# Optimization experiments

Measured on AMD Instinct MI355X. Metric: run time of the kernel, lower is better.

The kernel has to match this reference:

```python
import jax, jax.numpy as jnp
import numpy as np

IN_F, OUT_F, EDGE_D = 128, 128, 16
B, S, E = 16, 1024, 8192
T = 1.0
NEG_SLOPE = 0.2


def setup_inputs() -> dict:
    key = jax.random.key(0)
    k1, k2, k3, k4, k5 = jax.random.split(key, 5)
    x = jax.random.normal(k1, (B, S, IN_F), dtype=jnp.float32)
    edge_index = jax.random.randint(k2, (B, E, 2), 0, S)
    edge_attr = jax.random.normal(k3, (B, E, EDGE_D), dtype=jnp.float32)
    node_mask = jnp.zeros((B, S), dtype=bool)   # all nodes valid
    edge_mask = jnp.zeros((B, E), dtype=bool)   # all edges valid
    # Xavier-uniform params
    limW = float(np.sqrt(6.0 / (IN_F + OUT_F)))
    W = jax.random.uniform(k4, (IN_F, OUT_F), minval=-limW, maxval=limW, dtype=jnp.float32)
    lima = float(np.sqrt(6.0 / (2 * OUT_F + EDGE_D + 1)))
    a = jax.random.uniform(k5, (2 * OUT_F + EDGE_D, 1), minval=-lima, maxval=lima, dtype=jnp.float32)
    return {"x": x, "edge_index": edge_index, "edge_attr": edge_attr,
            "node_mask": node_mask, "edge_mask": edge_mask, "W": W, "a": a}


def reference(x, edge_index, edge_attr, node_mask, edge_mask, W, a):
    # All masks are all-valid, so global node id = b*S + n (identity compaction).
    Bs, Ss, _ = x.shape
    Es = edge_index.shape[1]
    N = Bs * Ss
    offs = (jnp.arange(Bs, dtype=edge_index.dtype) * Ss)[:, None]      # [B,1]
    src = (edge_index[..., 0] + offs).reshape(-1)                      # [B*E]
    dst = (edge_index[..., 1] + offs).reshape(-1)
    ea = edge_attr.reshape(-1, edge_attr.shape[-1])                    # [B*E, D_e]
    # undirected: add reverse edges
    src2 = jnp.concatenate([src, dst])
    dst2 = jnp.concatenate([dst, src])
    ea2 = jnp.concatenate([ea, ea], axis=0)
    # self-loops with zero edge attr
    nodes = jnp.arange(N, dtype=src.dtype)
    src_all = jnp.concatenate([src2, nodes])                           # [M]
    dst_all = jnp.concatenate([dst2, nodes])
    ea_all = jnp.concatenate([ea2, jnp.zeros((N, ea.shape[-1]), ea.dtype)], axis=0)
    # node transform
    xt = (x @ W).reshape(N, -1)                                        # [N, out]
    h_src = xt[src_all]                                                # [M, out]
    h_dst = xt[dst_all]
    # per-edge attention logit: [h_src || h_dst || e_attr] @ a, leaky relu
    feats = jnp.concatenate([h_src, h_dst, ea_all], axis=-1)           # [M, 2*out+D_e]
    e = jax.nn.leaky_relu((feats @ a)[:, 0], NEG_SLOPE) / T            # [M]
    # segment softmax over destination nodes (every node has a self-loop)
    seg_max = jax.ops.segment_max(e, dst_all, num_segments=N)
    ex = jnp.exp(e - seg_max[dst_all])
    denom = jax.ops.segment_sum(ex, dst_all, num_segments=N)
    alpha = ex / denom[dst_all]                                        # [M]
    # weighted scatter-aggregate
    h_agg = jax.ops.segment_sum(alpha[:, None] * h_src, dst_all, num_segments=N)
    return h_agg.reshape(Bs, Ss, -1)
```

## Files before the change

kernel.cpp:

```cpp
#include <hip/hip_runtime.h>
#include <hip/hip_bf16.h>

constexpr int BB = 16;
constexpr int SS = 1024;
constexpr int EE = 8192;
constexpr int F  = 128;
constexpr int ED = 16;
constexpr int NN = BB * SS;
constexpr int BE = BB * EE;
constexpr int CAP = 64;
constexpr float NEG = 0.2f;

constexpr size_t OFF_XT    = 0;
constexpr size_t OFF_PSRC  = OFF_XT   + (size_t)NN * F * 4;
constexpr size_t OFF_PDST  = OFF_PSRC + (size_t)NN * 4;
constexpr size_t OFF_SLOG  = OFF_PDST + (size_t)NN * 4;
constexpr size_t OFF_MAXK  = OFF_SLOG + (size_t)NN * 4;
constexpr size_t OFF_CNT   = OFF_MAXK + (size_t)NN * 4;
constexpr size_t OFF_EDATA = OFF_CNT  + (size_t)NN * 4;

static __device__ __forceinline__ float leaky(float v) {
    return v > 0.0f ? v : NEG * v;
}
static __device__ __forceinline__ unsigned enc(float f) {
    unsigned u = __float_as_uint(f);
    return ((int)u < 0) ? ~u : (u | 0x80000000u);
}
static __device__ __forceinline__ float dec(unsigned k) {
    unsigned u = (k & 0x80000000u) ? (k & 0x7fffffffu) : ~k;
    return __uint_as_float(u);
}

__global__ __launch_bounds__(256) void k_gemm(const float* __restrict__ x,
                                              const float* __restrict__ W,
                                              const float* __restrict__ a,
                                              float* __restrict__ xt,
                                              float* __restrict__ p_src,
                                              float* __restrict__ p_dst,
                                              float* __restrict__ slog,
                                              unsigned* __restrict__ maxk,
                                              int* __restrict__ cnt) {
    __shared__ float xs[32 * 128];
    __shared__ float Wl[64 * 128];
    const int tid  = threadIdx.x;
    const int base = blockIdx.x * 32;

    if (tid < 32) cnt[base + tid] = 0;

    {
        const float4* x4 = (const float4*)(x + (size_t)base * F);
        float4* xs4 = (float4*)xs;
#pragma unroll
        for (int i = 0; i < 4; ++i) xs4[tid + 256 * i] = x4[tid + 256 * i];
    }

    const int rb = tid >> 5;
    const int fb = tid & 31;
    const int r0 = rb * 4;
    const int f0 = fb * 4;

    float4 acc[4];
#pragma unroll
    for (int r = 0; r < 4; ++r) acc[r] = make_float4(0.f, 0.f, 0.f, 0.f);

    for (int kb = 0; kb < 128; kb += 64) {
        __syncthreads();
        const float4* W4 = (const float4*)(W + (size_t)kb * F);
        float4* Wl4 = (float4*)Wl;
#pragma unroll
        for (int i = 0; i < 8; ++i) Wl4[tid + 256 * i] = W4[tid + 256 * i];
        __syncthreads();

        for (int k = 0; k < 64; k += 4) {
            float4 xv[4], wv[4];
#pragma unroll
            for (int r = 0; r < 4; ++r)
                xv[r] = *(const float4*)&xs[(r0 + r) * 128 + kb + k];
#pragma unroll
            for (int kk = 0; kk < 4; ++kk)
                wv[kk] = *(const float4*)&Wl[(k + kk) * 128 + f0];
#pragma unroll
            for (int r = 0; r < 4; ++r) {
                acc[r].x = fmaf(xv[r].x, wv[0].x, acc[r].x);
                acc[r].y = fmaf(xv[r].x, wv[0].y, acc[r].y);
                acc[r].z = fmaf(xv[r].x, wv[0].z, acc[r].z);
                acc[r].w = fmaf(xv[r].x, wv[0].w, acc[r].w);
                acc[r].x = fmaf(xv[r].y, wv[1].x, acc[r].x);
                acc[r].y = fmaf(xv[r].y, wv[1].y, acc[r].y);
                acc[r].z = fmaf(xv[r].y, wv[1].z, acc[r].z);
                acc[r].w = fmaf(xv[r].y, wv[1].w, acc[r].w);
                acc[r].x = fmaf(xv[r].z, wv[2].x, acc[r].x);
                acc[r].y = fmaf(xv[r].z, wv[2].y, acc[r].y);
                acc[r].z = fmaf(xv[r].z, wv[2].z, acc[r].z);
                acc[r].w = fmaf(xv[r].z, wv[2].w, acc[r].w);
                acc[r].x = fmaf(xv[r].w, wv[3].x, acc[r].x);
                acc[r].y = fmaf(xv[r].w, wv[3].y, acc[r].y);
                acc[r].z = fmaf(xv[r].w, wv[3].z, acc[r].z);
                acc[r].w = fmaf(xv[r].w, wv[3].w, acc[r].w);
            }
        }
    }

#pragma unroll
    for (int r = 0; r < 4; ++r)
        *(float4*)&xt[(size_t)(base + r0 + r) * F + f0] = acc[r];

    const float4 as4 = *(const float4*)&a[f0];
    const float4 ad4 = *(const float4*)&a[128 + f0];
    float ps[4], pd[4];
#pragma unroll
    for (int r = 0; r < 4; ++r) {
        ps[r] = acc[r].x * as4.x + acc[r].y * as4.y + acc[r].z * as4.z + acc[r].w * as4.w;
        pd[r] = acc[r].x * ad4.x + acc[r].y * ad4.y + acc[r].z * ad4.z + acc[r].w * ad4.w;
    }
#pragma unroll
    for (int off = 1; off <= 16; off <<= 1) {
#pragma unroll
        for (int r = 0; r < 4; ++r) {
            ps[r] += __shfl_xor(ps[r], off);
            pd[r] += __shfl_xor(pd[r], off);
        }
    }
    if ((tid & 31) == 0) {
#pragma unroll
        for (int r = 0; r < 4; ++r) {
            const int row = base + r0 + r;
            p_src[row] = ps[r];
            p_dst[row] = pd[r];
            const float sl = leaky(ps[r] + pd[r]);
            slog[row] = sl;
            maxk[row] = enc(sl);
        }
    }
}

__global__ __launch_bounds__(256) void k_scatter(const int* __restrict__ edge_index,
                                                 const float* __restrict__ edge_attr,
                                                 const float* __restrict__ a,
                                                 const float* __restrict__ p_src,
                                                 const float* __restrict__ p_dst,
                                                 int* __restrict__ cnt,
                                                 unsigned* __restrict__ maxk,
                                                 float2* __restrict__ edata) {
    const int bid = blockIdx.x;
    const int bid2 = ((bid & 7) << 6) | (bid >> 3);
    const int i = bid2 * 256 + threadIdx.x;
    const int2 sd = ((const int2*)edge_index)[i];
    const int off = (i >> 13) << 10;
    const int s = off + sd.x;
    const int d = off + sd.y;

    const float4* ea4 = (const float4*)(edge_attr + (size_t)i * ED);
    const float4* ae4 = (const float4*)(a + 256);
    float q = 0.0f;
#pragma unroll
    for (int j = 0; j < 4; ++j) {
        const float4 e = ea4[j];
        const float4 w = ae4[j];
        q = fmaf(e.x, w.x, fmaf(e.y, w.y, fmaf(e.z, w.z, fmaf(e.w, w.w, q))));
    }

    const float pss = p_src[s], pdd = p_dst[d];
    const float psd = p_src[d], pds = p_dst[s];
    const float l0 = leaky(pss + pdd + q);
    const float l1 = leaky(psd + pds + q);

    atomicMax(&maxk[d], enc(l0));
    atomicMax(&maxk[s], enc(l1));

    const int pos0 = atomicAdd(&cnt[d], 1);
    if (pos0 < CAP) edata[(size_t)d * CAP + pos0] = make_float2(__int_as_float(s), l0);
    const int pos1 = atomicAdd(&cnt[s], 1);
    if (pos1 < CAP) edata[(size_t)s * CAP + pos1] = make_float2(__int_as_float(d), l1);
}

__global__ __launch_bounds__(256) void k_agg(const float* __restrict__ xt,
                                             const float* __restrict__ slog,
                                             const unsigned* __restrict__ maxk,
                                             const int* __restrict__ cnt,
                                             const float2* __restrict__ edata,
                                             float* __restrict__ out) {
    const int wave = threadIdx.x >> 6;
    const int lane = threadIdx.x & 63;
    const int bid = blockIdx.x;
    const int bid2 = ((bid & 7) << 9) | (bid >> 3);
    const int d = bid2 * 4 + wave;
    const float2* xt2 = (const float2*)xt;

    const float2 ev = edata[(size_t)d * CAP + lane];
    const int n = min(cnt[d], CAP);
    const float m = dec(maxk[d]);
    const float wself = __expf(slog[d] - m);
    const float2 xd = xt2[(size_t)d * 64 + lane];
    float ax = wself * xd.x, ay = wself * xd.y;
    float l = wself;

    int j = 0;
    for (; j + 4 <= n; j += 4) {
        const float e0x = __shfl(ev.x, j + 0), e0y = __shfl(ev.y, j + 0);
        const float e1x = __shfl(ev.x, j + 1), e1y = __shfl(ev.y, j + 1);
        const float e2x = __shfl(ev.x, j + 2), e2y = __shfl(ev.y, j + 2);
        const float e3x = __shfl(ev.x, j + 3), e3y = __shfl(ev.y, j + 3);
        const float2 x0 = xt2[(size_t)__float_as_int(e0x) * 64 + lane];
        const float2 x1 = xt2[(size_t)__float_as_int(e1x) * 64 + lane];
        const float2 x2 = xt2[(size_t)__float_as_int(e2x) * 64 + lane];
        const float2 x3 = xt2[(size_t)__float_as_int(e3x) * 64 + lane];
        const float w0 = __expf(e0y - m);
        const float w1 = __expf(e1y - m);
        const float w2 = __expf(e2y - m);
        const float w3 = __expf(e3y - m);
        ax = fmaf(w0, x0.x, ax); ay = fmaf(w0, x0.y, ay);
        ax = fmaf(w1, x1.x, ax); ay = fmaf(w1, x1.y, ay);
        ax = fmaf(w2, x2.x, ax); ay = fmaf(w2, x2.y, ay);
        ax = fmaf(w3, x3.x, ax); ay = fmaf(w3, x3.y, ay);
        l += (w0 + w1) + (w2 + w3);
    }
    for (; j < n; ++j) {
        const float ex = __shfl(ev.x, j), ey = __shfl(ev.y, j);
        const float2 x0 = xt2[(size_t)__float_as_int(ex) * 64 + lane];
        const float w0 = __expf(ey - m);
        ax = fmaf(w0, x0.x, ax); ay = fmaf(w0, x0.y, ay);
        l += w0;
    }
    const float inv = 1.0f / l;
    ((float2*)out)[(size_t)d * 64 + lane] = make_float2(ax * inv, ay * inv);
}

extern "C" void kernel_launch(void* const* d_in, const int* in_sizes, int n_in,
                              void* d_out, int out_size, void* d_ws, size_t ws_size,
                              hipStream_t stream) {
    const float* x          = (const float*)d_in[0];
    const int*   edge_index = (const int*)d_in[1];
    const float* edge_attr  = (const float*)d_in[2];
    const float* W          = (const float*)d_in[5];
    const float* a          = (const float*)d_in[6];
    float* out = (float*)d_out;

    char* ws = (char*)d_ws;
    float*    xt    = (float*)(ws + OFF_XT);
    float*    p_src = (float*)(ws + OFF_PSRC);
    float*    p_dst = (float*)(ws + OFF_PDST);
    float*    slog  = (float*)(ws + OFF_SLOG);
    unsigned* maxk  = (unsigned*)(ws + OFF_MAXK);
    int*      cnt   = (int*)(ws + OFF_CNT);
    float2*   edata = (float2*)(ws + OFF_EDATA);

    k_gemm<<<NN / 32, 256, 0, stream>>>(x, W, a, xt, p_src, p_dst, slog, maxk, cnt);
    k_scatter<<<BE / 256, 256, 0, stream>>>(edge_index, edge_attr, a, p_src, p_dst, cnt, maxk, edata);
    k_agg<<<NN / 4, 256, 0, stream>>>(xt, slog, maxk, cnt, edata, out);
}
```

Baseline: 127.4 us.

## Fuse three phases into one cooperative kernel with grid syncs

Merges the gemm, scatter and aggregation kernels into a single cooperative launch of 512 persistent blocks, separated by grid-wide barriers, so the two inter-kernel launch gaps go away. The aggregation phase now handles 8 destination nodes per wave instead of one, and block-to-XCD mappings are recomputed for each phase. If the cooperative launch fails, it falls back to three separate launches. The cost is grid sync overhead, lower occupancy from the launch bounds of 2 blocks per CU, and less latency hiding in the gather-heavy aggregation phase.

```diff
diff --git a/kernel.cpp b/kernel.cpp
--- a/kernel.cpp
+++ b/kernel.cpp
@@ -1,5 +1,7 @@
 #include <hip/hip_runtime.h>
-#include <hip/hip_bf16.h>
+#include <hip/hip_cooperative_groups.h>
+
+namespace cg = cooperative_groups;
 
 constexpr int BB = 16;
 constexpr int SS = 1024;
@@ -11,6 +13,8 @@
 constexpr int CAP = 64;
 constexpr float NEG = 0.2f;
 
+constexpr int NBLK = 512;
+
 constexpr size_t OFF_XT    = 0;
 constexpr size_t OFF_PSRC  = OFF_XT   + (size_t)NN * F * 4;
 constexpr size_t OFF_PDST  = OFF_PSRC + (size_t)NN * 4;
@@ -31,19 +35,16 @@
     return __uint_as_float(u);
 }
 
-__global__ __launch_bounds__(256) void k_gemm(const float* __restrict__ x,
-                                              const float* __restrict__ W,
-                                              const float* __restrict__ a,
-                                              float* __restrict__ xt,
-                                              float* __restrict__ p_src,
-                                              float* __restrict__ p_dst,
-                                              float* __restrict__ slog,
-                                              unsigned* __restrict__ maxk,
-                                              int* __restrict__ cnt) {
-    __shared__ float xs[32 * 128];
-    __shared__ float Wl[64 * 128];
-    const int tid  = threadIdx.x;
-    const int base = blockIdx.x * 32;
+static __device__ __forceinline__ void phase_gemm(
+        int bid, int tid,
+        const float* __restrict__ x, const float* __restrict__ W,
+        const float* __restrict__ a,
+        float* __restrict__ xt, float* __restrict__ p_src, float* __restrict__ p_dst,
+        float* __restrict__ slog, unsigned* __restrict__ maxk, int* __restrict__ cnt,
+        float* xs, float* Wl) {
+    const int xcd = bid & 7;
+    const int j   = bid >> 3;
+    const int base = (xcd * 64 + j) * 32;
 
     if (tid < 32) cnt[base + tid] = 0;
 
@@ -134,17 +135,15 @@
     }
 }
 
-__global__ __launch_bounds__(256) void k_scatter(const int* __restrict__ edge_index,
-                                                 const float* __restrict__ edge_attr,
-                                                 const float* __restrict__ a,
-                                                 const float* __restrict__ p_src,
-                                                 const float* __restrict__ p_dst,
-                                                 int* __restrict__ cnt,
-                                                 unsigned* __restrict__ maxk,
-                                                 float2* __restrict__ edata) {
-    const int bid = blockIdx.x;
-    const int bid2 = ((bid & 7) << 6) | (bid >> 3);
-    const int i = bid2 * 256 + threadIdx.x;
+static __device__ __forceinline__ void phase_scatter(
+        int bid, int tid,
+        const int* __restrict__ edge_index, const float* __restrict__ edge_attr,
+        const float* __restrict__ a,
+        const float* __restrict__ p_src, const float* __restrict__ p_dst,
+        int* __restrict__ cnt, unsigned* __restrict__ maxk, float2* __restrict__ edata) {
+    const int xcd = bid & 7;
+    const int j   = bid >> 3;
+    const int i = (xcd * 64 + j) * 256 + tid;
     const int2 sd = ((const int2*)edge_index)[i];
     const int off = (i >> 13) << 10;
     const int s = off + sd.x;
@@ -154,9 +153,9 @@
     const float4* ae4 = (const float4*)(a + 256);
     float q = 0.0f;
 #pragma unroll
-    for (int j = 0; j < 4; ++j) {
-        const float4 e = ea4[j];
-        const float4 w = ae4[j];
+    for (int jj = 0; jj < 4; ++jj) {
+        const float4 e = ea4[jj];
+        const float4 w = ae4[jj];
         q = fmaf(e.x, w.x, fmaf(e.y, w.y, fmaf(e.z, w.z, fmaf(e.w, w.w, q))));
     }
 
@@ -174,56 +173,98 @@
     if (pos1 < CAP) edata[(size_t)s * CAP + pos1] = make_float2(__int_as_float(d), l1);
 }
 
-__global__ __launch_bounds__(256) void k_agg(const float* __restrict__ xt,
-                                             const float* __restrict__ slog,
-                                             const unsigned* __restrict__ maxk,
-                                             const int* __restrict__ cnt,
-                                             const float2* __restrict__ edata,
-                                             float* __restrict__ out) {
-    const int wave = threadIdx.x >> 6;
-    const int lane = threadIdx.x & 63;
-    const int bid = blockIdx.x;
-    const int bid2 = ((bid & 7) << 9) | (bid >> 3);
-    const int d = bid2 * 4 + wave;
+static __device__ __forceinline__ void phase_agg(
+        int bid, int tid,
+        const float* __restrict__ xt, const float* __restrict__ slog,
+        const unsigned* __restrict__ maxk, const int* __restrict__ cnt,
+        const float2* __restrict__ edata, float* __restrict__ out) {
+    const int xcd  = bid & 7;
+    const int j    = bid >> 3;
+    const int wv   = tid >> 6;
+    const int lane = tid & 63;
+    const int w    = j * 4 + wv;
+    const int d0   = xcd * 2048 + w * 8;
     const float2* xt2 = (const float2*)xt;
 
-    const float2 ev = edata[(size_t)d * CAP + lane];
-    const int n = min(cnt[d], CAP);
-    const float m = dec(maxk[d]);
-    const float wself = __expf(slog[d] - m);
-    const float2 xd = xt2[(size_t)d * 64 + lane];
-    float ax = wself * xd.x, ay = wself * xd.y;
-    float l = wself;
-
-    int j = 0;
-    for (; j + 4 <= n; j += 4) {
-        const float e0x = __shfl(ev.x, j + 0), e0y = __shfl(ev.y, j + 0);
-        const float e1x = __shfl(ev.x, j + 1), e1y = __shfl(ev.y, j + 1);
-        const float e2x = __shfl(ev.x, j + 2), e2y = __shfl(ev.y, j + 2);
-        const float e3x = __shfl(ev.x, j + 3), e3y = __shfl(ev.y, j + 3);
-        const float2 x0 = xt2[(size_t)__float_as_int(e0x) * 64 + lane];
-        const float2 x1 = xt2[(size_t)__float_as_int(e1x) * 64 + lane];
-        const float2 x2 = xt2[(size_t)__float_as_int(e2x) * 64 + lane];
-        const float2 x3 = xt2[(size_t)__float_as_int(e3x) * 64 + lane];
-        const float w0 = __expf(e0y - m);
-        const float w1 = __expf(e1y - m);
-        const float w2 = __expf(e2y - m);
-        const float w3 = __expf(e3y - m);
-        ax = fmaf(w0, x0.x, ax); ay = fmaf(w0, x0.y, ay);
-        ax = fmaf(w1, x1.x, ax); ay = fmaf(w1, x1.y, ay);
-        ax = fmaf(w2, x2.x, ax); ay = fmaf(w2, x2.y, ay);
-        ax = fmaf(w3, x3.x, ax); ay = fmaf(w3, x3.y, ay);
-        l += (w0 + w1) + (w2 + w3);
-    }
-    for (; j < n; ++j) {
-        const float ex = __shfl(ev.x, j), ey = __shfl(ev.y, j);
-        const float2 x0 = xt2[(size_t)__float_as_int(ex) * 64 + lane];
-        const float w0 = __expf(ey - m);
-        ax = fmaf(w0, x0.x, ax); ay = fmaf(w0, x0.y, ay);
-        l += w0;
-    }
-    const float inv = 1.0f / l;
-    ((float2*)out)[(size_t)d * 64 + lane] = make_float2(ax * inv, ay * inv);
+    for (int d = d0; d < d0 + 8; ++d) {
+        const float2 ev = edata[(size_t)d * CAP + lane];
+        const int n = min(cnt[d], CAP);
+        const float m = dec(maxk[d]);
+        const float wself = __expf(slog[d] - m);
+        const float2 xd = xt2[(size_t)d * 64 + lane];
+        float ax = wself * xd.x, ay = wself * xd.y;
+        float l = wself;
+
+        int k = 0;
+        for (; k + 4 <= n; k += 4) {
+            const float e0x = __shfl(ev.x, k + 0), e0y = __shfl(ev.y, k + 0);
+            const float e1x = __shfl(ev.x, k + 1), e1y = __shfl(ev.y, k + 1);
+            const float e2x = __shfl(ev.x, k + 2), e2y = __shfl(ev.y, k + 2);
+            const float e3x = __shfl(ev.x, k + 3), e3y = __shfl(ev.y, k + 3);
+            const float2 x0 = xt2[(size_t)__float_as_int(e0x) * 64 + lane];
+            const float2 x1 = xt2[(size_t)__float_as_int(e1x) * 64 + lane];
+            const float2 x2 = xt2[(size_t)__float_as_int(e2x) * 64 + lane];
+            const float2 x3 = xt2[(size_t)__float_as_int(e3x) * 64 + lane];
+            const float w0 = __expf(e0y - m);
+            const float w1 = __expf(e1y - m);
+            const float w2 = __expf(e2y - m);
+            const float w3 = __expf(e3y - m);
+            ax = fmaf(w0, x0.x, ax); ay = fmaf(w0, x0.y, ay);
+            ax = fmaf(w1, x1.x, ax); ay = fmaf(w1, x1.y, ay);
+            ax = fmaf(w2, x2.x, ax); ay = fmaf(w2, x2.y, ay);
+            ax = fmaf(w3, x3.x, ax); ay = fmaf(w3, x3.y, ay);
+            l += (w0 + w1) + (w2 + w3);
+        }
+        for (; k < n; ++k) {
+            const float ex = __shfl(ev.x, k), ey = __shfl(ev.y, k);
+            const float2 x0 = xt2[(size_t)__float_as_int(ex) * 64 + lane];
+            const float w0 = __expf(ey - m);
+            ax = fmaf(w0, x0.x, ax); ay = fmaf(w0, x0.y, ay);
+            l += w0;
+        }
+        const float inv = 1.0f / l;
+        ((float2*)out)[(size_t)d * 64 + lane] = make_float2(ax * inv, ay * inv);
+    }
+}
+
+__global__ __launch_bounds__(256, 2) void k_fused(
+        const float* __restrict__ x, const float* __restrict__ W,
+        const float* __restrict__ a,
+        const int* __restrict__ edge_index, const float* __restrict__ edge_attr,
+        float* __restrict__ xt, float* __restrict__ p_src, float* __restrict__ p_dst,
+        float* __restrict__ slog, unsigned* __restrict__ maxk, int* __restrict__ cnt,
+        float2* __restrict__ edata, float* __restrict__ out) {
+    cg::grid_group grid = cg::this_grid();
+    __shared__ float xs[32 * 128];
+    __shared__ float Wl[64 * 128];
+    phase_gemm(blockIdx.x, threadIdx.x, x, W, a, xt, p_src, p_dst, slog, maxk, cnt, xs, Wl);
+    grid.sync();
+    phase_scatter(blockIdx.x, threadIdx.x, edge_index, edge_attr, a, p_src, p_dst, cnt, maxk, edata);
+    grid.sync();
+    phase_agg(blockIdx.x, threadIdx.x, xt, slog, maxk, cnt, edata, out);
+}
+
+__global__ __launch_bounds__(256) void k_gemm_s(
+        const float* __restrict__ x, const float* __restrict__ W,
+        const float* __restrict__ a,
+        float* __restrict__ xt, float* __restrict__ p_src, float* __restrict__ p_dst,
+        float* __restrict__ slog, unsigned* __restrict__ maxk, int* __restrict__ cnt) {
+    __shared__ float xs[32 * 128];
+    __shared__ float Wl[64 * 128];
+    phase_gemm(blockIdx.x, threadIdx.x, x, W, a, xt, p_src, p_dst, slog, maxk, cnt, xs, Wl);
+}
+__global__ __launch_bounds__(256) void k_scatter_s(
+        const int* __restrict__ edge_index, const float* __restrict__ edge_attr,
+        const float* __restrict__ a,
+        const float* __restrict__ p_src, const float* __restrict__ p_dst,
+        int* __restrict__ cnt, unsigned* __restrict__ maxk, float2* __restrict__ edata) {
+    phase_scatter(blockIdx.x, threadIdx.x, edge_index, edge_attr, a, p_src, p_dst, cnt, maxk, edata);
+}
+__global__ __launch_bounds__(256) void k_agg_s(
+        const float* __restrict__ xt, const float* __restrict__ slog,
+        const unsigned* __restrict__ maxk, const int* __restrict__ cnt,
+        const float2* __restrict__ edata, float* __restrict__ out) {
+    phase_agg(blockIdx.x, threadIdx.x, xt, slog, maxk, cnt, edata, out);
 }
 
 extern "C" void kernel_launch(void* const* d_in, const int* in_sizes, int n_in,
@@ -245,7 +286,15 @@
     int*      cnt   = (int*)(ws + OFF_CNT);
     float2*   edata = (float2*)(ws + OFF_EDATA);
 
-    k_gemm<<<NN / 32, 256, 0, stream>>>(x, W, a, xt, p_src, p_dst, slog, maxk, cnt);
-    k_scatter<<<BE / 256, 256, 0, stream>>>(edge_index, edge_attr, a, p_src, p_dst, cnt, maxk, edata);
-    k_agg<<<NN / 4, 256, 0, stream>>>(xt, slog, maxk, cnt, edata, out);
-}
+    void* args[] = { (void*)&x, (void*)&W, (void*)&a, (void*)&edge_index, (void*)&edge_attr,
+                     (void*)&xt, (void*)&p_src, (void*)&p_dst, (void*)&slog,
+                     (void*)&maxk, (void*)&cnt, (void*)&edata, (void*)&out };
+    hipError_t err = hipLaunchCooperativeKernel((const void*)k_fused,
+                                                dim3(NBLK), dim3(256), args, 0, stream);
+    if (err != hipSuccess) {
+        (void)hipGetLastError();
+        k_gemm_s<<<NBLK, 256, 0, stream>>>(x, W, a, xt, p_src, p_dst, slog, maxk, cnt);
+        k_scatter_s<<<NBLK, 256, 0, stream>>>(edge_index, edge_attr, a, p_src, p_dst, cnt, maxk, edata);
+        k_agg_s<<<NBLK, 256, 0, stream>>>(xt, slog, maxk, cnt, edata, out);
+    }
+}
```

Result: slower. 271.4 us (+113.0%).
